# Performance work log

Measured on AMD Instinct MI355X. Metric: run time of the kernel, lower is better.

Reference implementation:

```python
import jax, jax.numpy as jnp
import numpy as np

NUM_HEADS = 4
GROUPS = 16
EPS = 1e-5


def setup_inputs() -> dict:
    key = jax.random.key(0)
    ks = jax.random.split(key, 7)
    b, c, hh, ww = 4, 256, 64, 64
    x = jax.random.normal(ks[0], (b, c, hh, ww), dtype=jnp.float32)
    norm_w = 1.0 + 0.1 * jax.random.normal(ks[1], (c,), dtype=jnp.float32)
    norm_b = 0.1 * jax.random.normal(ks[2], (c,), dtype=jnp.float32)
    qkv_w = jax.random.normal(ks[3], (3 * c, c), dtype=jnp.float32) / np.sqrt(c)
    qkv_b = 0.01 * jax.random.normal(ks[4], (3 * c,), dtype=jnp.float32)
    # NOTE: original zero-inits proj_out; we use random weights so the
    # attention path actually affects the output (kernel correctness test).
    proj_w = jax.random.normal(ks[5], (c, c), dtype=jnp.float32) / np.sqrt(c)
    proj_b = jnp.zeros((c,), dtype=jnp.float32)
    return {"x": x, "norm_w": norm_w, "norm_b": norm_b,
            "qkv_w": qkv_w, "qkv_b": qkv_b,
            "proj_w": proj_w, "proj_b": proj_b}


def _group_norm(x, w, b):
    # x: [B, C, T]; GroupNorm32 computes in fp32 (inputs already fp32)
    B, C, T = x.shape
    xg = x.reshape(B, GROUPS, C // GROUPS, T)
    mean = jnp.mean(xg, axis=(2, 3), keepdims=True)
    var = jnp.var(xg, axis=(2, 3), keepdims=True)
    xn = ((xg - mean) * jax.lax.rsqrt(var + EPS)).reshape(B, C, T)
    return xn * w[None, :, None] + b[None, :, None]


def reference(x, norm_w, norm_b, qkv_w, qkv_b, proj_w, proj_b):
    b, c = x.shape[0], x.shape[1]
    spatial = x.shape[2:]
    x2 = x.reshape(b, c, -1)                       # [B, C, T]
    T = x2.shape[-1]
    normed = _group_norm(x2, norm_w, norm_b)
    qkv = jnp.einsum('oc,bct->bot', qkv_w, normed) + qkv_b[None, :, None]
    # faithful reshape: [B, 3C, T] -> [B*H, 3C/H, T], then split in thirds
    qkv = qkv.reshape(b * NUM_HEADS, (3 * c) // NUM_HEADS, T)
    ch = qkv.shape[1] // 3                         # = C / H
    q, k, v = jnp.split(qkv, 3, axis=1)
    scale = 1.0 / np.sqrt(np.sqrt(ch))
    weight = jnp.einsum('bct,bcs->bts', q * scale, k * scale)
    weight = jax.nn.softmax(weight.astype(jnp.float32), axis=-1).astype(qkv.dtype)
    h = jnp.einsum('bts,bcs->bct', weight, v)      # [B*H, ch, T]
    h = h.reshape(b, c, T)
    h = jnp.einsum('oc,bct->bot', proj_w, h) + proj_b[None, :, None]
    return (x2 + h).reshape(b, c, *spatial)
```

## Files before the change

kernel.cpp:

```cpp
#include <hip/hip_runtime.h>

constexpr int kB  = 4;
constexpr int kC  = 256;
constexpr int kT  = 4096;
constexpr int kG  = 16;
constexpr int kCg = kC / kG;
constexpr int kH  = 4;
constexpr int kCh = kC / kH;
constexpr float kEps = 1e-5f;
constexpr float kQScale = 0.125f * 1.4426950408889634f;

typedef short bf16x8 __attribute__((ext_vector_type(8)));
typedef float f32x4  __attribute__((ext_vector_type(4)));
typedef float f32x16 __attribute__((ext_vector_type(16)));

__device__ inline unsigned short f2bf(float f) {
    union { float f; unsigned u; } v; v.f = f;
    unsigned r = v.u + 0x7fffu + ((v.u >> 16) & 1u);
    return (unsigned short)(r >> 16);
}
__device__ inline unsigned pk2bf(float a, float b) {
    return (unsigned)f2bf(a) | ((unsigned)f2bf(b) << 16);
}
__device__ inline unsigned pk2bf_trunc(float a, float b) {
    return __builtin_amdgcn_perm(__float_as_uint(b), __float_as_uint(a), 0x07060302u);
}

__global__ __launch_bounds__(256) void gn_stats_kernel(const float* __restrict__ x,
                                                       float* __restrict__ stats) {
    int bg = blockIdx.x;
    const float4* xp4 = (const float4*)(x + (size_t)bg * (kCg * kT));
    int tid = threadIdx.x;
    float s = 0.f, q = 0.f;
    #pragma unroll 4
    for (int i = 0; i < (kCg * kT / 4) / 256; ++i) {
        float4 v = xp4[tid + i * 256];
        s += v.x + v.y + v.z + v.w;
        q += v.x * v.x + v.y * v.y + v.z * v.z + v.w * v.w;
    }
    #pragma unroll
    for (int off = 32; off > 0; off >>= 1) {
        s += __shfl_down(s, off);
        q += __shfl_down(q, off);
    }
    __shared__ float rs[4], rq[4];
    int wid = tid >> 6, lane = tid & 63;
    if (lane == 0) { rs[wid] = s; rq[wid] = q; }
    __syncthreads();
    if (tid == 0) {
        float S = rs[0] + rs[1] + rs[2] + rs[3];
        float Q = rq[0] + rq[1] + rq[2] + rq[3];
        const float invN = 1.0f / (float)(kCg * kT);
        float mean = S * invN;
        float var  = Q * invN - mean * mean;
        stats[bg * 2 + 0] = mean;
        stats[bg * 2 + 1] = rsqrtf(var + kEps);
    }
}

__global__ __launch_bounds__(256) void gn_apply_t_kernel(const float* __restrict__ x,
                                                         const float* __restrict__ stats,
                                                         const float* __restrict__ w,
                                                         const float* __restrict__ bias,
                                                         unsigned short* __restrict__ normT) {
    __shared__ float Ls[64][65];
    int t0 = blockIdx.x * 64;
    int c0 = blockIdx.y * 64;
    int b  = blockIdx.z;
    int tid = threadIdx.x;
    #pragma unroll
    for (int p = 0; p < 4; ++p) {
        int idx = tid + p * 256;
        int cl = idx >> 4, t4 = idx & 15;
        int c = c0 + cl;
        int bg = b * kG + (c >> 4);
        float mean = stats[bg * 2 + 0];
        float rstd = stats[bg * 2 + 1];
        float sw = w[c] * rstd;
        float sb = bias[c] - mean * sw;
        float4 v = *(const float4*)&x[((size_t)b * kC + c) * kT + t0 + t4 * 4];
        Ls[t4 * 4 + 0][cl] = v.x * sw + sb;
        Ls[t4 * 4 + 1][cl] = v.y * sw + sb;
        Ls[t4 * 4 + 2][cl] = v.z * sw + sb;
        Ls[t4 * 4 + 3][cl] = v.w * sw + sb;
    }
    __syncthreads();
    {
        int row = tid >> 2, cq = (tid & 3) * 16;
        unsigned tmp[8];
        #pragma unroll
        for (int i = 0; i < 8; ++i)
            tmp[i] = pk2bf(Ls[row][cq + 2 * i], Ls[row][cq + 2 * i + 1]);
        uint4* dst = (uint4*)&normT[((size_t)b * kT + t0 + row) * kC + c0 + cq];
        dst[0] = make_uint4(tmp[0], tmp[1], tmp[2], tmp[3]);
        dst[1] = make_uint4(tmp[4], tmp[5], tmp[6], tmp[7]);
    }
}

__global__ __launch_bounds__(256) void wcvt_kernel(const float* __restrict__ qkv_w,
                                                   const float* __restrict__ proj_w,
                                                   unsigned short* __restrict__ wbf) {
    int gid = blockIdx.x * 256 + threadIdx.x;
    for (int i = gid; i < 65536; i += gridDim.x * 256) {
        float4 v = (i < 49152) ? ((const float4*)qkv_w)[i]
                               : ((const float4*)proj_w)[i - 49152];
        *(uint2*)&wbf[(size_t)i * 4] = make_uint2(pk2bf(v.x, v.y), pk2bf(v.z, v.w));
    }
}

__global__ __launch_bounds__(256) void qkv_gemm_kernel(const unsigned short* __restrict__ wbf,
                                                       const float* __restrict__ qkv_b,
                                                       const unsigned short* __restrict__ normT,
                                                       unsigned short* __restrict__ qTg,
                                                       unsigned short* __restrict__ kTg,
                                                       unsigned short* __restrict__ vCg) {
    constexpr int LDK = 72;
    constexpr int LDV = 136;
    __shared__ __align__(16) unsigned short As[64 * LDK];
    __shared__ __align__(16) unsigned short Bs[128 * LDK];

    int t0 = blockIdx.x * 128;
    int m0 = blockIdx.y * 64;
    int b  = blockIdx.z;
    const unsigned short* Ab = wbf + (size_t)m0 * kC;
    const unsigned short* Bb = normT + (size_t)b * kT * kC;

    int tid = threadIdx.x;
    int wave = tid >> 6, lane = tid & 63;
    int ln15 = lane & 15, quad = lane >> 4;
    int wm = wave >> 1, wt = wave & 1;

    f32x4 acc[2][4] = {};

    for (int k0 = 0; k0 < kC; k0 += 64) {
        __syncthreads();
        #pragma unroll
        for (int p = 0; p < 2; ++p) {
            int idx = tid + p * 256;
            int row = idx >> 3, seg = idx & 7;
            *(uint4*)&As[row * LDK + seg * 8] =
                *(const uint4*)&Ab[(size_t)row * kC + k0 + seg * 8];
        }
        #pragma unroll
        for (int p = 0; p < 4; ++p) {
            int idx = tid + p * 256;
            int row = idx >> 3, seg = idx & 7;
            *(uint4*)&Bs[row * LDK + seg * 8] =
                *(const uint4*)&Bb[(size_t)(t0 + row) * kC + k0 + seg * 8];
        }
        __syncthreads();
        #pragma unroll
        for (int ks = 0; ks < 2; ++ks) {
            bf16x8 af[2], bf[4];
            #pragma unroll
            for (int i = 0; i < 2; ++i)
                af[i] = *(bf16x8*)&As[(wm * 32 + i * 16 + ln15) * LDK + ks * 32 + quad * 8];
            #pragma unroll
            for (int j = 0; j < 4; ++j)
                bf[j] = *(bf16x8*)&Bs[(wt * 64 + j * 16 + ln15) * LDK + ks * 32 + quad * 8];
            #pragma unroll
            for (int i = 0; i < 2; ++i)
                #pragma unroll
                for (int j = 0; j < 4; ++j)
                    acc[i][j] = __builtin_amdgcn_mfma_f32_16x16x32_bf16(
                        af[i], bf[j], acc[i][j], 0, 0, 0);
        }
    }

    int type = (m0 % 192) / 64;
    int h = m0 / 192;
    int bh = b * kH + h;
    __syncthreads();
    #pragma unroll
    for (int i = 0; i < 2; ++i) {
        float4 bv = *(const float4*)&qkv_b[m0 + wm * 32 + i * 16 + quad * 4];
        const float* bp = (const float*)&bv;
        #pragma unroll
        for (int j = 0; j < 4; ++j) {
            int tl = wt * 64 + j * 16 + ln15;
            int c = wm * 32 + i * 16 + quad * 4;
            float v0 = acc[i][j][0] + bp[0];
            float v1 = acc[i][j][1] + bp[1];
            float v2 = acc[i][j][2] + bp[2];
            float v3 = acc[i][j][3] + bp[3];
            if (type == 0) {
                v0 *= kQScale; v1 *= kQScale; v2 *= kQScale; v3 *= kQScale;
            }
            if (type != 2) {
                *(uint2*)&Bs[tl * LDK + c] = make_uint2(pk2bf(v0, v1), pk2bf(v2, v3));
            } else {
                Bs[(c + 0) * LDV + tl] = f2bf(v0);
                Bs[(c + 1) * LDV + tl] = f2bf(v1);
                Bs[(c + 2) * LDV + tl] = f2bf(v2);
                Bs[(c + 3) * LDV + tl] = f2bf(v3);
            }
        }
    }
    __syncthreads();
    if (type != 2) {
        unsigned short* base = ((type == 0) ? qTg : kTg) + (size_t)bh * (kT * kCh);
        #pragma unroll
        for (int p = 0; p < 4; ++p) {
            int f = tid + p * 256;
            int ln = f & 31, hif = (f >> 5) & 1, ks = (f >> 6) & 3, tb = f >> 8;
            *(uint4*)&base[((t0 >> 5) + tb) * 2048 + ks * 512 + hif * 256 + ln * 8] =
                *(uint4*)&Bs[(tb * 32 + ln) * LDK + ks * 16 + hif * 8];
        }
    } else {
        unsigned short* base = vCg + (size_t)bh * (kT * kCh);
        #pragma unroll
        for (int p = 0; p < 4; ++p) {
            int f = tid + p * 256;
            int c = f & 63, hif = (f >> 6) & 1, sg = f >> 7;
            *(uint4*)&base[((t0 >> 4) + sg) * 1024 + hif * 512 + c * 8] =
                *(uint4*)&Bs[c * LDV + sg * 16 + hif * 8];
        }
    }
}

__global__ __launch_bounds__(256, 4) void attn_mfma_kernel(const unsigned short* __restrict__ qTg,
                                                           const unsigned short* __restrict__ kTg,
                                                           const unsigned short* __restrict__ vCg,
                                                           unsigned short* __restrict__ attnT) {
    constexpr int LDK = 72;
    __shared__ __align__(16) unsigned short Ps[64 * LDK];
    __shared__ float l_part[2][64];

    int bh = blockIdx.y;
    int t0 = blockIdx.x * 64;
    int b = bh >> 2, h = bh & 3;

    int tid = threadIdx.x;
    int wave = tid >> 6, lane = tid & 63;
    int ln31 = lane & 31, hi = lane >> 5;
    int sh = wave >> 1, th = wave & 1;

    const unsigned short* qb = qTg + (size_t)bh * (kT * kCh);
    const unsigned short* kb = kTg + (size_t)bh * (kT * kCh);
    const unsigned short* vb = vCg + (size_t)bh * (kT * kCh);

    bf16x8 qf[4];
    {
        const unsigned short* qp = qb + ((t0 >> 5) + th) * 2048 + hi * 256 + ln31 * 8;
        #pragma unroll
        for (int ks = 0; ks < 4; ++ks) qf[ks] = *(const bf16x8*)(qp + ks * 512);
    }
    const unsigned short* kptr = kb + sh * 2048 + hi * 256 + ln31 * 8;
    const unsigned short* vptr = vb + hi * 512 + (sh * 32 + ln31) * 8;

    bf16x8 kf[4], vf[4];
    #pragma unroll
    for (int ks = 0; ks < 4; ++ks) kf[ks] = *(const bf16x8*)(kptr + ks * 512);
    #pragma unroll
    for (int ks = 0; ks < 4; ++ks) vf[ks] = *(const bf16x8*)(vptr + ks * 1024);

    float l_r = 0.f;
    f32x16 accO = {};

    for (int s0 = 0; s0 < kT; s0 += 64) {
        f32x16 accS = {};
        #pragma unroll
        for (int ks = 0; ks < 4; ++ks)
            accS = __builtin_amdgcn_mfma_f32_32x32x16_bf16(kf[ks], qf[ks], accS, 0, 0, 0);

        if (s0 + 64 < kT) {
            kptr += 4096;
            #pragma unroll
            for (int ks = 0; ks < 4; ++ks) kf[ks] = *(const bf16x8*)(kptr + ks * 512);
        }

        int t = th * 32 + ln31;
        float rs = 0.f;
        #pragma unroll
        for (int g = 0; g < 4; ++g) {
            float p0 = __builtin_amdgcn_exp2f(accS[4 * g + 0]);
            float p1 = __builtin_amdgcn_exp2f(accS[4 * g + 1]);
            float p2 = __builtin_amdgcn_exp2f(accS[4 * g + 2]);
            float p3 = __builtin_amdgcn_exp2f(accS[4 * g + 3]);
            rs += (p0 + p1) + (p2 + p3);
            *(uint2*)&Ps[t * LDK + sh * 32 + 8 * g + 4 * hi] =
                make_uint2(pk2bf_trunc(p0, p1), pk2bf_trunc(p2, p3));
        }
        rs += __shfl_xor(rs, 32);
        l_r += rs;
        __syncthreads();

        #pragma unroll
        for (int ks = 0; ks < 4; ++ks) {
            bf16x8 pf = *(bf16x8*)&Ps[(th * 32 + ln31) * LDK + ks * 16 + hi * 8];
            accO = __builtin_amdgcn_mfma_f32_32x32x16_bf16(vf[ks], pf, accO, 0, 0, 0);
        }

        if (s0 + 64 < kT) {
            vptr += 4096;
            #pragma unroll
            for (int ks = 0; ks < 4; ++ks) vf[ks] = *(const bf16x8*)(vptr + ks * 1024);
        }
        __syncthreads();
    }

    if (hi == 0) l_part[sh][th * 32 + ln31] = l_r;
    __syncthreads();
    int t = th * 32 + ln31;
    float linv = 1.0f / (l_part[0][t] + l_part[1][t]);
    #pragma unroll
    for (int g = 0; g < 4; ++g) {
        int c = sh * 32 + 8 * g + 4 * hi;
        float v0 = accO[4 * g + 0] * linv;
        float v1 = accO[4 * g + 1] * linv;
        float v2 = accO[4 * g + 2] * linv;
        float v3 = accO[4 * g + 3] * linv;
        *(uint2*)&attnT[((size_t)b * kT + t0 + t) * kC + h * kCh + c] =
            make_uint2(pk2bf(v0, v1), pk2bf(v2, v3));
    }
}

__global__ __launch_bounds__(256) void proj_gemm_kernel(const unsigned short* __restrict__ wpbf,
                                                        const float* __restrict__ proj_b,
                                                        const unsigned short* __restrict__ attnT,
                                                        const float* __restrict__ x,
                                                        float* __restrict__ out) {
    constexpr int LDK = 72;
    __shared__ __align__(16) unsigned short As[64 * LDK];
    __shared__ __align__(16) unsigned short Bs[128 * LDK];

    int t0 = blockIdx.x * 128;
    int m0 = blockIdx.y * 64;
    int b  = blockIdx.z;
    const unsigned short* Ab = wpbf + (size_t)m0 * kC;
    const unsigned short* Bb = attnT + (size_t)b * kT * kC;

    int tid = threadIdx.x;
    int wave = tid >> 6, lane = tid & 63;
    int ln15 = lane & 15, quad = lane >> 4;
    int wm = wave >> 1, wt = wave & 1;

    f32x4 acc[2][4] = {};

    for (int k0 = 0; k0 < kC; k0 += 64) {
        __syncthreads();
        #pragma unroll
        for (int p = 0; p < 2; ++p) {
            int idx = tid + p * 256;
            int row = idx >> 3, seg = idx & 7;
            *(uint4*)&As[row * LDK + seg * 8] =
                *(const uint4*)&Ab[(size_t)row * kC + k0 + seg * 8];
        }
        #pragma unroll
        for (int p = 0; p < 4; ++p) {
            int idx = tid + p * 256;
            int row = idx >> 3, seg = idx & 7;
            *(uint4*)&Bs[row * LDK + seg * 8] =
                *(const uint4*)&Bb[(size_t)(t0 + row) * kC + k0 + seg * 8];
        }
        __syncthreads();
        #pragma unroll
        for (int ks = 0; ks < 2; ++ks) {
            bf16x8 af[2], bf[4];
            #pragma unroll
            for (int i = 0; i < 2; ++i)
                af[i] = *(bf16x8*)&As[(wm * 32 + i * 16 + ln15) * LDK + ks * 32 + quad * 8];
            #pragma unroll
            for (int j = 0; j < 4; ++j)
                bf[j] = *(bf16x8*)&Bs[(wt * 64 + j * 16 + ln15) * LDK + ks * 32 + quad * 8];
            #pragma unroll
            for (int i = 0; i < 2; ++i)
                #pragma unroll
                for (int j = 0; j < 4; ++j)
                    acc[i][j] = __builtin_amdgcn_mfma_f32_16x16x32_bf16(
                        af[i], bf[j], acc[i][j], 0, 0, 0);
        }
    }

    #pragma unroll
    for (int i = 0; i < 2; ++i) {
        float4 bv = *(const float4*)&proj_b[m0 + wm * 32 + i * 16 + quad * 4];
        const float* bp = (const float*)&bv;
        #pragma unroll
        for (int j = 0; j < 4; ++j) {
            int t = t0 + wt * 64 + j * 16 + ln15;
            int mbase = m0 + wm * 32 + i * 16 + quad * 4;
            #pragma unroll
            for (int r = 0; r < 4; ++r) {
                size_t off = ((size_t)b * kC + mbase + r) * kT + t;
                out[off] = acc[i][j][r] + bp[r] + x[off];
            }
        }
    }
}

extern "C" void kernel_launch(void* const* d_in, const int* in_sizes, int n_in,
                              void* d_out, int out_size, void* d_ws, size_t ws_size,
                              hipStream_t stream) {
    const float* x      = (const float*)d_in[0];
    const float* norm_w = (const float*)d_in[1];
    const float* norm_b = (const float*)d_in[2];
    const float* qkv_w  = (const float*)d_in[3];
    const float* qkv_b  = (const float*)d_in[4];
    const float* proj_w = (const float*)d_in[5];
    const float* proj_b = (const float*)d_in[6];
    float* out = (float*)d_out;

    float* stats = (float*)d_ws;
    unsigned short* wsbf  = (unsigned short*)((float*)d_ws + 128);
    unsigned short* normT = wsbf;
    unsigned short* wbf   = normT + (size_t)kB * kT * kC;
    unsigned short* qTp   = wbf + 262144;
    unsigned short* kTp   = qTp + (size_t)kB * kH * kT * kCh;
    unsigned short* vCp   = kTp + (size_t)kB * kH * kT * kCh;
    unsigned short* attnT = vCp + (size_t)kB * kH * kT * kCh;
    unsigned short* wpbf  = wbf + 196608;

    gn_stats_kernel<<<kB * kG, 256, 0, stream>>>(x, stats);
    gn_apply_t_kernel<<<dim3(kT / 64, kC / 64, kB), 256, 0, stream>>>(
        x, stats, norm_w, norm_b, normT);
    wcvt_kernel<<<128, 256, 0, stream>>>(qkv_w, proj_w, wbf);
    qkv_gemm_kernel<<<dim3(kT / 128, 12, kB), 256, 0, stream>>>(
        wbf, qkv_b, normT, qTp, kTp, vCp);
    attn_mfma_kernel<<<dim3(kT / 64, kB * kH), 256, 0, stream>>>(qTp, kTp, vCp, attnT);
    proj_gemm_kernel<<<dim3(kT / 128, kC / 64, kB), 256, 0, stream>>>(
        wpbf, proj_b, attnT, x, out);
}
```

Before: 218.5 us.

## Merge prep kernels, register-prefetch GEMM tiles, widen attention key block to 128

New measurement: 247.8 us. +13.4%, slower.

```diff
diff --git a/kernel.cpp b/kernel.cpp
--- a/kernel.cpp
+++ b/kernel.cpp
@@ -26,11 +26,23 @@
     return __builtin_amdgcn_perm(__float_as_uint(b), __float_as_uint(a), 0x07060302u);
 }
 
-__global__ __launch_bounds__(256) void gn_stats_kernel(const float* __restrict__ x,
-                                                       float* __restrict__ stats) {
+__global__ __launch_bounds__(256) void prep_kernel(const float* __restrict__ x,
+                                                   float* __restrict__ stats,
+                                                   const float* __restrict__ qkv_w,
+                                                   const float* __restrict__ proj_w,
+                                                   unsigned short* __restrict__ wbf) {
+    int tid = threadIdx.x;
+    if (blockIdx.x >= 64) {
+        int gid = (blockIdx.x - 64) * 256 + tid;
+        for (int i = gid; i < 65536; i += 128 * 256) {
+            float4 v = (i < 49152) ? ((const float4*)qkv_w)[i]
+                                   : ((const float4*)proj_w)[i - 49152];
+            *(uint2*)&wbf[(size_t)i * 4] = make_uint2(pk2bf(v.x, v.y), pk2bf(v.z, v.w));
+        }
+        return;
+    }
     int bg = blockIdx.x;
     const float4* xp4 = (const float4*)(x + (size_t)bg * (kCg * kT));
-    int tid = threadIdx.x;
     float s = 0.f, q = 0.f;
     #pragma unroll 4
     for (int i = 0; i < (kCg * kT / 4) / 256; ++i) {
@@ -97,17 +109,6 @@
     }
 }
 
-__global__ __launch_bounds__(256) void wcvt_kernel(const float* __restrict__ qkv_w,
-                                                   const float* __restrict__ proj_w,
-                                                   unsigned short* __restrict__ wbf) {
-    int gid = blockIdx.x * 256 + threadIdx.x;
-    for (int i = gid; i < 65536; i += gridDim.x * 256) {
-        float4 v = (i < 49152) ? ((const float4*)qkv_w)[i]
-                               : ((const float4*)proj_w)[i - 49152];
-        *(uint2*)&wbf[(size_t)i * 4] = make_uint2(pk2bf(v.x, v.y), pk2bf(v.z, v.w));
-    }
-}
-
 __global__ __launch_bounds__(256) void qkv_gemm_kernel(const unsigned short* __restrict__ wbf,
                                                        const float* __restrict__ qkv_b,
                                                        const unsigned short* __restrict__ normT,
@@ -130,25 +131,34 @@
     int ln15 = lane & 15, quad = lane >> 4;
     int wm = wave >> 1, wt = wave & 1;
 
+    int arow = tid >> 3, aseg = tid & 7;
     f32x4 acc[2][4] = {};
+    uint4 Ar[2], Br[4];
+
+    #pragma unroll
+    for (int p = 0; p < 2; ++p)
+        Ar[p] = *(const uint4*)&Ab[(size_t)(arow + p * 32) * kC + aseg * 8];
+    #pragma unroll
+    for (int p = 0; p < 4; ++p)
+        Br[p] = *(const uint4*)&Bb[(size_t)(t0 + arow + p * 32) * kC + aseg * 8];
 
     for (int k0 = 0; k0 < kC; k0 += 64) {
+        if (k0) __syncthreads();
+        #pragma unroll
+        for (int p = 0; p < 2; ++p)
+            *(uint4*)&As[(arow + p * 32) * LDK + aseg * 8] = Ar[p];
+        #pragma unroll
+        for (int p = 0; p < 4; ++p)
+            *(uint4*)&Bs[(arow + p * 32) * LDK + aseg * 8] = Br[p];
         __syncthreads();
-        #pragma unroll
-        for (int p = 0; p < 2; ++p) {
-            int idx = tid + p * 256;
-            int row = idx >> 3, seg = idx & 7;
-            *(uint4*)&As[row * LDK + seg * 8] =
-                *(const uint4*)&Ab[(size_t)row * kC + k0 + seg * 8];
-        }
-        #pragma unroll
-        for (int p = 0; p < 4; ++p) {
-            int idx = tid + p * 256;
-            int row = idx >> 3, seg = idx & 7;
-            *(uint4*)&Bs[row * LDK + seg * 8] =
-                *(const uint4*)&Bb[(size_t)(t0 + row) * kC + k0 + seg * 8];
-        }
-        __syncthreads();
+        if (k0 + 64 < kC) {
+            #pragma unroll
+            for (int p = 0; p < 2; ++p)
+                Ar[p] = *(const uint4*)&Ab[(size_t)(arow + p * 32) * kC + k0 + 64 + aseg * 8];
+            #pragma unroll
+            for (int p = 0; p < 4; ++p)
+                Br[p] = *(const uint4*)&Bb[(size_t)(t0 + arow + p * 32) * kC + k0 + 64 + aseg * 8];
+        }
         #pragma unroll
         for (int ks = 0; ks < 2; ++ks) {
             bf16x8 af[2], bf[4];
@@ -218,12 +228,12 @@
     }
 }
 
-__global__ __launch_bounds__(256, 4) void attn_mfma_kernel(const unsigned short* __restrict__ qTg,
+__global__ __launch_bounds__(256, 3) void attn_mfma_kernel(const unsigned short* __restrict__ qTg,
                                                            const unsigned short* __restrict__ kTg,
                                                            const unsigned short* __restrict__ vCg,
                                                            unsigned short* __restrict__ attnT) {
-    constexpr int LDK = 72;
-    __shared__ __align__(16) unsigned short Ps[64 * LDK];
+    constexpr int LDP = 136;
+    __shared__ __align__(16) unsigned short Ps[64 * LDP];
     __shared__ float l_part[2][64];
 
     int bh = blockIdx.y;
@@ -248,37 +258,53 @@
     const unsigned short* kptr = kb + sh * 2048 + hi * 256 + ln31 * 8;
     const unsigned short* vptr = vb + hi * 512 + (sh * 32 + ln31) * 8;
 
-    bf16x8 kf[4], vf[4];
-    #pragma unroll
-    for (int ks = 0; ks < 4; ++ks) kf[ks] = *(const bf16x8*)(kptr + ks * 512);
-    #pragma unroll
-    for (int ks = 0; ks < 4; ++ks) vf[ks] = *(const bf16x8*)(vptr + ks * 1024);
+    bf16x8 kf[8], vf[8];
+    #pragma unroll
+    for (int i = 0; i < 8; ++i)
+        kf[i] = *(const bf16x8*)(kptr + (i >> 2) * 4096 + (i & 3) * 512);
+    #pragma unroll
+    for (int i = 0; i < 8; ++i)
+        vf[i] = *(const bf16x8*)(vptr + i * 1024);
 
     float l_r = 0.f;
     f32x16 accO = {};
 
-    for (int s0 = 0; s0 < kT; s0 += 64) {
-        f32x16 accS = {};
+    for (int s0 = 0; s0 < kT; s0 += 128) {
+        f32x16 accS0 = {}, accS1 = {};
         #pragma unroll
         for (int ks = 0; ks < 4; ++ks)
-            accS = __builtin_amdgcn_mfma_f32_32x32x16_bf16(kf[ks], qf[ks], accS, 0, 0, 0);
-
-        if (s0 + 64 < kT) {
-            kptr += 4096;
-            #pragma unroll
-            for (int ks = 0; ks < 4; ++ks) kf[ks] = *(const bf16x8*)(kptr + ks * 512);
+            accS0 = __builtin_amdgcn_mfma_f32_32x32x16_bf16(kf[ks], qf[ks], accS0, 0, 0, 0);
+        #pragma unroll
+        for (int ks = 0; ks < 4; ++ks)
+            accS1 = __builtin_amdgcn_mfma_f32_32x32x16_bf16(kf[4 + ks], qf[ks], accS1, 0, 0, 0);
+
+        if (s0 + 128 < kT) {
+            kptr += 8192;
+            #pragma unroll
+            for (int i = 0; i < 8; ++i)
+                kf[i] = *(const bf16x8*)(kptr + (i >> 2) * 4096 + (i & 3) * 512);
         }
 
         int t = th * 32 + ln31;
         float rs = 0.f;
         #pragma unroll
         for (int g = 0; g < 4; ++g) {
-            float p0 = __builtin_amdgcn_exp2f(accS[4 * g + 0]);
-            float p1 = __builtin_amdgcn_exp2f(accS[4 * g + 1]);
-            float p2 = __builtin_amdgcn_exp2f(accS[4 * g + 2]);
-            float p3 = __builtin_amdgcn_exp2f(accS[4 * g + 3]);
+            float p0 = __builtin_amdgcn_exp2f(accS0[4 * g + 0]);
+            float p1 = __builtin_amdgcn_exp2f(accS0[4 * g + 1]);
+            float p2 = __builtin_amdgcn_exp2f(accS0[4 * g + 2]);
+            float p3 = __builtin_amdgcn_exp2f(accS0[4 * g + 3]);
             rs += (p0 + p1) + (p2 + p3);
-            *(uint2*)&Ps[t * LDK + sh * 32 + 8 * g + 4 * hi] =
+            *(uint2*)&Ps[t * LDP + sh * 32 + 8 * g + 4 * hi] =
+                make_uint2(pk2bf_trunc(p0, p1), pk2bf_trunc(p2, p3));
+        }
+        #pragma unroll
+        for (int g = 0; g < 4; ++g) {
+            float p0 = __builtin_amdgcn_exp2f(accS1[4 * g + 0]);
+            float p1 = __builtin_amdgcn_exp2f(accS1[4 * g + 1]);
+            float p2 = __builtin_amdgcn_exp2f(accS1[4 * g + 2]);
+            float p3 = __builtin_amdgcn_exp2f(accS1[4 * g + 3]);
+            rs += (p0 + p1) + (p2 + p3);
+            *(uint2*)&Ps[t * LDP + 64 + sh * 32 + 8 * g + 4 * hi] =
                 make_uint2(pk2bf_trunc(p0, p1), pk2bf_trunc(p2, p3));
         }
         rs += __shfl_xor(rs, 32);
@@ -286,15 +312,16 @@
         __syncthreads();
 
         #pragma unroll
-        for (int ks = 0; ks < 4; ++ks) {
-            bf16x8 pf = *(bf16x8*)&Ps[(th * 32 + ln31) * LDK + ks * 16 + hi * 8];
-            accO = __builtin_amdgcn_mfma_f32_32x32x16_bf16(vf[ks], pf, accO, 0, 0, 0);
-        }
-
-        if (s0 + 64 < kT) {
-            vptr += 4096;
-            #pragma unroll
-            for (int ks = 0; ks < 4; ++ks) vf[ks] = *(const bf16x8*)(vptr + ks * 1024);
+        for (int i = 0; i < 8; ++i) {
+            bf16x8 pf = *(bf16x8*)&Ps[(th * 32 + ln31) * LDP + i * 16 + hi * 8];
+            accO = __builtin_amdgcn_mfma_f32_32x32x16_bf16(vf[i], pf, accO, 0, 0, 0);
+        }
+
+        if (s0 + 128 < kT) {
+            vptr += 8192;
+            #pragma unroll
+            for (int i = 0; i < 8; ++i)
+                vf[i] = *(const bf16x8*)(vptr + i * 1024);
         }
         __syncthreads();
     }
@@ -335,25 +362,34 @@
     int ln15 = lane & 15, quad = lane >> 4;
     int wm = wave >> 1, wt = wave & 1;
 
+    int arow = tid >> 3, aseg = tid & 7;
     f32x4 acc[2][4] = {};
+    uint4 Ar[2], Br[4];
+
+    #pragma unroll
+    for (int p = 0; p < 2; ++p)
+        Ar[p] = *(const uint4*)&Ab[(size_t)(arow + p * 32) * kC + aseg * 8];
+    #pragma unroll
+    for (int p = 0; p < 4; ++p)
+        Br[p] = *(const uint4*)&Bb[(size_t)(t0 + arow + p * 32) * kC + aseg * 8];
 
     for (int k0 = 0; k0 < kC; k0 += 64) {
+        if (k0) __syncthreads();
+        #pragma unroll
+        for (int p = 0; p < 2; ++p)
+            *(uint4*)&As[(arow + p * 32) * LDK + aseg * 8] = Ar[p];
+        #pragma unroll
+        for (int p = 0; p < 4; ++p)
+            *(uint4*)&Bs[(arow + p * 32) * LDK + aseg * 8] = Br[p];
         __syncthreads();
-        #pragma unroll
-        for (int p = 0; p < 2; ++p) {
-            int idx = tid + p * 256;
-            int row = idx >> 3, seg = idx & 7;
-            *(uint4*)&As[row * LDK + seg * 8] =
-                *(const uint4*)&Ab[(size_t)row * kC + k0 + seg * 8];
-        }
-        #pragma unroll
-        for (int p = 0; p < 4; ++p) {
-            int idx = tid + p * 256;
-            int row = idx >> 3, seg = idx & 7;
-            *(uint4*)&Bs[row * LDK + seg * 8] =
-                *(const uint4*)&Bb[(size_t)(t0 + row) * kC + k0 + seg * 8];
-        }
-        __syncthreads();
+        if (k0 + 64 < kC) {
+            #pragma unroll
+            for (int p = 0; p < 2; ++p)
+                Ar[p] = *(const uint4*)&Ab[(size_t)(arow + p * 32) * kC + k0 + 64 + aseg * 8];
+            #pragma unroll
+            for (int p = 0; p < 4; ++p)
+                Br[p] = *(const uint4*)&Bb[(size_t)(t0 + arow + p * 32) * kC + k0 + 64 + aseg * 8];
+        }
         #pragma unroll
         for (int ks = 0; ks < 2; ++ks) {
             bf16x8 af[2], bf[4];
@@ -411,10 +447,9 @@
     unsigned short* attnT = vCp + (size_t)kB * kH * kT * kCh;
     unsigned short* wpbf  = wbf + 196608;
 
-    gn_stats_kernel<<<kB * kG, 256, 0, stream>>>(x, stats);
+    prep_kernel<<<192, 256, 0, stream>>>(x, stats, qkv_w, proj_w, wbf);
     gn_apply_t_kernel<<<dim3(kT / 64, kC / 64, kB), 256, 0, stream>>>(
         x, stats, norm_w, norm_b, normT);
-    wcvt_kernel<<<128, 256, 0, stream>>>(qkv_w, proj_w, wbf);
     qkv_gemm_kernel<<<dim3(kT / 128, 12, kB), 256, 0, stream>>>(
         wbf, qkv_b, normT, qTp, kTp, vCp);
     attn_mfma_kernel<<<dim3(kT / 64, kB * kH), 256, 0, stream>>>(qTp, kTp, vCp, attnT);
```
